# Kernel optimization log

Hardware: AMD Instinct MI355X
Metric: run time of the kernel (lower is better)

The kernel has to match this reference:

```python
import jax, jax.numpy as jnp
import numpy as np

NUM_HEADS = 8
CH_PER_HEAD = 32
NUM_GROUPS = 32
EPS = 1e-5
SCALE = CH_PER_HEAD ** (-0.25)


def group_norm(x, scale, bias):
    # x: [b, c, h, w]
    b, c, h, w = x.shape
    xg = x.reshape(b, NUM_GROUPS, c // NUM_GROUPS, h, w)
    mean = xg.mean(axis=(2, 3, 4), keepdims=True)
    var = xg.var(axis=(2, 3, 4), keepdims=True)
    xg = (xg - mean) * jax.lax.rsqrt(var + EPS)
    x = xg.reshape(b, c, h, w)
    return x * scale[None, :, None, None] + bias[None, :, None, None]


def conv1x1(x, w, b):
    # x: [b, c_in, n], w: [c_out, c_in], b: [c_out]
    return jnp.einsum('oc,bcn->bon', w, x) + b[None, :, None]


def setup_inputs() -> dict:
    key = jax.random.key(0)
    ks = jax.random.split(key, 12)
    c_in, c_out, hid = 256, 256, NUM_HEADS * CH_PER_HEAD
    d = {}
    d['x'] = jax.random.normal(ks[0], (2, c_in, 64, 64), dtype=jnp.float32)
    d['gn_scale'] = jnp.ones((c_in,), dtype=jnp.float32)
    d['gn_bias'] = jnp.zeros((c_in,), dtype=jnp.float32)
    def lin(k, co, ci):
        return jax.random.normal(k, (co, ci), dtype=jnp.float32) * (ci ** -0.5)
    d['wq'] = lin(ks[1], hid, c_in)
    d['bq'] = jnp.zeros((hid,), dtype=jnp.float32)
    d['wk'] = lin(ks[2], hid, c_in)
    d['bk'] = jnp.zeros((hid,), dtype=jnp.float32)
    d['wv'] = lin(ks[3], hid, c_in)
    d['bv'] = jnp.zeros((hid,), dtype=jnp.float32)
    # Original zero-inits to_out; we use small random weights so the
    # attention path contributes to the output (non-trivial baseline).
    d['wo'] = lin(ks[4], c_out, hid) * 0.02
    d['bo'] = jnp.zeros((c_out,), dtype=jnp.float32)
    return d


def reference(x, gn_scale, gn_bias, wq, bq, wk, bk, wv, bv, wo, bo):
    b, c, h, w = x.shape
    n = h * w
    x_n = group_norm(x, gn_scale, gn_bias).reshape(b, c, n)
    q = conv1x1(x_n, wq, bq)  # [b, hid, n]
    k = conv1x1(x_n, wk, bk)
    v = conv1x1(x_n, wv, bv)
    def split_heads(t):
        return t.reshape(b, NUM_HEADS, CH_PER_HEAD, n)
    q, k, v = split_heads(q) * SCALE, split_heads(k) * SCALE, split_heads(v)
    attn = jax.nn.softmax(jnp.einsum('bhdi,bhdj->bhij', q, k), axis=-1)
    out = jnp.einsum('bhij,bhdj->bhdi', attn, v)  # [b, h, d, n]
    out = out.reshape(b, NUM_HEADS * CH_PER_HEAD, n)
    out = conv1x1(out, wo, bo).reshape(b, -1, h, w)
    return x + out
```

## Files before the change

### kernel.cpp

```cpp
#include <hip/hip_runtime.h>

#define C 256
#define N 4096
#define CPG 8
#define GE (CPG * N)
#define JL 2048

constexpr float EPS = 1e-5f;
constexpr float QK_SCALE_E = 0.50500979f;

typedef float f32x4 __attribute__((ext_vector_type(4)));
typedef short s16x8 __attribute__((ext_vector_type(8)));

__device__ __forceinline__ short f2bf(float f) {
    union { float f; unsigned u; } v; v.f = f;
    unsigned r = v.u + 0x7FFFu + ((v.u >> 16) & 1u);
    return (short)(r >> 16);
}
__device__ __forceinline__ float bf2f(short s) {
    union { unsigned u; float f; } v; v.u = ((unsigned)(unsigned short)s) << 16;
    return v.f;
}

__global__ __launch_bounds__(256) void k_stats(const float* __restrict__ x,
                                               float2* __restrict__ partials) {
    int q = blockIdx.x & 3, g = (blockIdx.x >> 2) & 31, b = blockIdx.x >> 7;
    size_t base = (size_t)(b * C + g * CPG) * N + q * (GE / 4);
    const float* xp = x + base;
    int tid = threadIdx.x;
    float sum = 0.f, ss = 0.f;
    for (int i = tid * 4; i < GE / 4; i += 1024) {
        float4 v = *(const float4*)(xp + i);
        sum += (v.x + v.y) + (v.z + v.w);
        ss  += (v.x * v.x + v.y * v.y) + (v.z * v.z + v.w * v.w);
    }
    #pragma unroll
    for (int o = 32; o; o >>= 1) {
        sum += __shfl_down(sum, o, 64);
        ss  += __shfl_down(ss, o, 64);
    }
    __shared__ float red[8];
    int wid = tid >> 6;
    if ((tid & 63) == 0) { red[wid] = sum; red[4 + wid] = ss; }
    __syncthreads();
    if (tid == 0) {
        sum = red[0] + red[1] + red[2] + red[3];
        ss  = red[4] + red[5] + red[6] + red[7];
        partials[(b * 32 + g) * 4 + q] = make_float2(sum, ss);
    }
}

__global__ __launch_bounds__(256) void k_wcvt(const float* __restrict__ wq,
        const float* __restrict__ wk, const float* __restrict__ wv,
        const float* __restrict__ wo, short* __restrict__ wqkvb,
        short* __restrict__ wob) {
    int i = blockIdx.x * 256 + threadIdx.x;
    if (i < 65536)       wqkvb[i] = f2bf(wq[i]);
    else if (i < 131072) wqkvb[i] = f2bf(wk[i - 65536]);
    else if (i < 196608) wqkvb[i] = f2bf(wv[i - 131072]);
    else                 wob[i - 196608] = f2bf(wo[i - 196608]);
}

__global__ __launch_bounds__(256) void k_t(const float* __restrict__ x,
        const float* __restrict__ gs, const float* __restrict__ gb,
        const float2* __restrict__ partials, short* __restrict__ xnT) {
    __shared__ __align__(16) short lt[64][72];
    int id = blockIdx.x;
    int b  = id >> 8;
    int ct = (id >> 6) & 3;
    int nt = id & 63;
    int c0 = ct * 64, n0 = nt * 64;
    int t = threadIdx.x;
    int cc = t >> 2;
    int c = c0 + cc;
    int bg = b * 32 + (c >> 3);
    float2 p0 = partials[bg * 4 + 0], p1 = partials[bg * 4 + 1];
    float2 p2 = partials[bg * 4 + 2], p3 = partials[bg * 4 + 3];
    float sum = (p0.x + p1.x) + (p2.x + p3.x);
    float ss  = (p0.y + p1.y) + (p2.y + p3.y);
    float mean = sum * (1.f / GE);
    float var  = ss * (1.f / GE) - mean * mean;
    float rstd = rsqrtf(var + EPS);
    float sc = gs[c] * rstd;
    float bi = gb[c] - mean * sc;
    const float* xp = x + (size_t)(b * C + c) * N + n0;
    #pragma unroll
    for (int it = 0; it < 4; ++it) {
        int f4 = (t & 3) + it * 4;
        float4 v = *(const float4*)(xp + f4 * 4);
        int nl = f4 * 4;
        lt[nl + 0][cc] = f2bf(v.x * sc + bi);
        lt[nl + 1][cc] = f2bf(v.y * sc + bi);
        lt[nl + 2][cc] = f2bf(v.z * sc + bi);
        lt[nl + 3][cc] = f2bf(v.w * sc + bi);
    }
    __syncthreads();
    int nl = t >> 2, seg = t & 3;
    short* op = xnT + (size_t)(b * N + n0 + nl) * C + c0 + seg * 16;
    s16x8 w0 = *(const s16x8*)&lt[nl][seg * 16];
    s16x8 w1 = *(const s16x8*)&lt[nl][seg * 16 + 8];
    *(s16x8*)op = w0;
    *(s16x8*)(op + 8) = w1;
}

__global__ __launch_bounds__(256) void k_qkv(const short* __restrict__ wqkvb,
        const short* __restrict__ xnT, const float* __restrict__ bq,
        const float* __restrict__ bk, const float* __restrict__ bv,
        short* __restrict__ qT, short* __restrict__ kT, short* __restrict__ vB) {
    __shared__ __align__(16) short bs[64 * 256];
    __shared__ __align__(16) short lt[4][64][16];
    int mb = blockIdx.x, nb = blockIdx.y, b = blockIdx.z;
    int m0 = mb * 64, n0 = nb * 64;
    int t = threadIdx.x;
    int wid = t >> 6, lane = t & 63;
    int lr = lane & 15, lg = lane >> 4;
    int mw = m0 + wid * 16;

    const short* ap_ = wqkvb + (mw + lr) * C + lg * 8;
    s16x8 af[8];
    #pragma unroll
    for (int kk = 0; kk < 8; ++kk)
        af[kk] = *(const s16x8*)(ap_ + kk * 32);

    {
        int gr = t >> 2;
        const short* gp = xnT + ((size_t)b * N + n0 + gr) * C + (t & 3) * 8;
        #pragma unroll
        for (int i = 0; i < 8; ++i) {
            int sl = (t & 3) + 4 * i;
            s16x8 v = *(const s16x8*)(gp + 32 * i);
            *(s16x8*)&bs[gr * 256 + ((sl ^ (gr & 7)) * 8)] = v;
        }
    }
    __syncthreads();

    f32x4 acc[4] = {{0,0,0,0},{0,0,0,0},{0,0,0,0},{0,0,0,0}};
    #pragma unroll
    for (int kk = 0; kk < 8; ++kk) {
        int sb = kk * 4;
        #pragma unroll
        for (int f = 0; f < 4; ++f) {
            int row = f * 16 + lr;
            s16x8 xf = *(const s16x8*)&bs[row * 256 + (((sb + lg) ^ (lr & 7)) * 8)];
            acc[f] = __builtin_amdgcn_mfma_f32_16x16x32_bf16(af[kk], xf, acc[f], 0, 0, 0);
        }
    }

    int kind = mb >> 2;
    const float* bias = kind == 0 ? bq : (kind == 1 ? bk : bv);
    int mloc = mw - kind * 256;
    float bvals[4];
    #pragma unroll
    for (int r = 0; r < 4; ++r) bvals[r] = bias[mloc + 4 * lg + r];
    int h = mloc >> 5;
    if (kind == 2) {
        short (*vt)[64] = (short(*)[64])lt;
        #pragma unroll
        for (int f = 0; f < 4; ++f)
            #pragma unroll
            for (int r = 0; r < 4; ++r) {
                int rl = wid * 16 + 4 * lg + r;
                int cn = f * 16 + lr;
                int sl = cn >> 3, off = cn & 7;
                vt[rl][((sl ^ (rl & 7)) * 8) + off] = f2bf(acc[f][r] + bvals[r]);
            }
        __syncthreads();
        int mlocB = mb * 64 - 512;
        int h0 = mlocB >> 5;
        int rr = t >> 2, sl = t & 3;
        int h2 = h0 + (rr >> 5), dd = rr & 31;
        short* vdst = vB + ((size_t)((b * 8 + h2) * 32 + dd)) * N + n0;
        s16x8 w0v = *(const s16x8*)&vt[rr][(sl ^ (rr & 7)) * 8];
        s16x8 w1v = *(const s16x8*)&vt[rr][((sl + 4) ^ (rr & 7)) * 8];
        *(s16x8*)(vdst + sl * 8) = w0v;
        *(s16x8*)(vdst + (sl + 4) * 8) = w1v;
    } else {
        short* dst = (kind == 0) ? qT : kT;
        #pragma unroll
        for (int f = 0; f < 4; ++f)
            #pragma unroll
            for (int r = 0; r < 4; ++r)
                lt[wid][f * 16 + lr][4 * lg + r] =
                    f2bf((acc[f][r] + bvals[r]) * QK_SCALE_E);
        int ln = lane;
        s16x8 w0 = *(const s16x8*)&lt[wid][ln][0];
        s16x8 w1 = *(const s16x8*)&lt[wid][ln][8];
        short* op = dst + ((size_t)(b * 8 + h) * N + n0 + ln) * 32 + (mloc & 16);
        *(s16x8*)op = w0;
        *(s16x8*)(op + 8) = w1;
    }
}

#define EXPB(d, s_) asm("v_exp_f32 %0, %1\n\ts_nop 0" : "=v"(d) : "v"(s_))

#define TILE_BODY() do {                                                          \
    f32x4 s0 = __builtin_amdgcn_mfma_f32_16x16x32_bf16(bk0, aq, zero, 0, 0, 0);   \
    f32x4 s1 = __builtin_amdgcn_mfma_f32_16x16x32_bf16(bk1, aq, zero, 0, 0, 0);   \
    float e00, e01, e02, e03, e10, e11, e12, e13;                                 \
    EXPB(e00, s0[0]); EXPB(e01, s0[1]); EXPB(e02, s0[2]); EXPB(e03, s0[3]);       \
    EXPB(e10, s1[0]); EXPB(e11, s1[1]); EXPB(e12, s1[2]); EXPB(e13, s1[3]);       \
    unsigned w0, w1, w2, w3;                                                      \
    asm("v_cvt_pk_bf16_f32 %0, %1, %2" : "=v"(w0) : "v"(e00), "v"(e01));          \
    asm("v_cvt_pk_bf16_f32 %0, %1, %2" : "=v"(w1) : "v"(e02), "v"(e03));          \
    asm("v_cvt_pk_bf16_f32 %0, %1, %2" : "=v"(w2) : "v"(e10), "v"(e11));          \
    asm("v_cvt_pk_bf16_f32 %0, %1, %2" : "=v"(w3) : "v"(e12), "v"(e13));          \
    asm("v_permlane32_swap_b32 %0, %1" : "+v"(w0), "+v"(w2));                     \
    asm("v_permlane16_swap_b32 %0, %1" : "+v"(w0), "+v"(w2));                     \
    asm("v_permlane32_swap_b32 %0, %1" : "+v"(w1), "+v"(w3));                     \
    asm("v_permlane16_swap_b32 %0, %1" : "+v"(w1), "+v"(w3));                     \
    union { int4 i4; s16x8 s8; } apu;                                             \
    apu.i4 = make_int4((int)w0, (int)w1, (int)w2, (int)w3);                       \
    s16x8 ap = apu.s8;                                                            \
    lac = __builtin_amdgcn_mfma_f32_16x16x32_bf16(ap, ones, lac, 0, 0, 0);        \
    o0  = __builtin_amdgcn_mfma_f32_16x16x32_bf16(ap, bv0, o0, 0, 0, 0);          \
    o1  = __builtin_amdgcn_mfma_f32_16x16x32_bf16(ap, bv1, o1, 0, 0, 0);          \
} while (0)

__global__ __launch_bounds__(256, 8) void k_attn(const short* __restrict__ qT,
        const short* __restrict__ kT, const short* __restrict__ vB,
        short* __restrict__ po0, short* __restrict__ po1,
        float* __restrict__ pl) {
    __shared__ __align__(16) short pool[8192];
    int xb  = blockIdx.x;
    int rm  = (xb & 7) * 128 + (xb >> 3);
    int bh  = rm >> 6;
    int wid = threadIdx.x >> 6;
    int i0  = (rm & 63) * 64 + wid * 16;
    int s   = blockIdx.y;
    int jb  = s * JL;
    int lane = threadIdx.x & 63;
    int lr = lane & 15, lg = lane >> 4;
    const short* qTb = qT + (size_t)bh * N * 32;
    const short* kTb = kT + (size_t)bh * N * 32;
    const short* vBb = vB + (size_t)bh * 32 * N;

    s16x8 aq = *(const s16x8*)(qTb + (i0 + lr) * 32 + lg * 8);
    s16x8 ones;
    #pragma unroll
    for (int e = 0; e < 8; ++e) ones[e] = (short)0x3F80;

    f32x4 o0 = {0,0,0,0}, o1 = {0,0,0,0}, lac = {0,0,0,0};
    const f32x4 zero = {0,0,0,0};

    int krow  = 16 * wid + (lane >> 2);
    int kslot = lane & 3;
    const short* kg = kTb + (size_t)(jb + krow) * 32 + kslot * 8;
    int kw_ofs = krow * 32 + ((kslot ^ (krow & 3)) * 8);

    int vrow  = 8 * wid + (lane >> 3);
    int vslot = lane & 7;
    const short* vg = vBb + (size_t)vrow * N + jb + vslot * 8;
    int vw_ofs = vrow * 64 + ((vslot ^ (vrow & 7)) * 8);

    int kr_base = lr * 32 + ((lg ^ (lr & 3)) * 8);
    int vr0 = lr * 64, vr1 = (16 + lr) * 64;
    int sw0 = ((0 + lg) ^ (lr & 7)) * 8;
    int sw1 = ((4 + lg) ^ (lr & 7)) * 8;

    {
        s16x8 kreg = *(const s16x8*)kg;
        s16x8 vreg = *(const s16x8*)vg;
        *(s16x8*)&pool[kw_ofs] = kreg;
        *(s16x8*)&pool[4096 + vw_ofs] = vreg;
    }
    __syncthreads();

    for (int t = 0; t < 32; ++t) {
        int p = t & 1;
        s16x8 nk, nv;
        if (t < 31) {
            nk = *(const s16x8*)(kg + (t + 1) * 2048);
            nv = *(const s16x8*)(vg + (t + 1) * 64);
        }
        const short* lkp = &pool[p * 2048];
        const short* lvp = &pool[4096 + p * 2048];
        {
            s16x8 bk0 = *(const s16x8*)(lkp + kr_base);
            s16x8 bk1 = *(const s16x8*)(lkp + 512 + kr_base);
            s16x8 bv0 = *(const s16x8*)(lvp + vr0 + sw0);
            s16x8 bv1 = *(const s16x8*)(lvp + vr1 + sw0);
            TILE_BODY();
        }
        {
            s16x8 bk0 = *(const s16x8*)(lkp + 1024 + kr_base);
            s16x8 bk1 = *(const s16x8*)(lkp + 1536 + kr_base);
            s16x8 bv0 = *(const s16x8*)(lvp + vr0 + sw1);
            s16x8 bv1 = *(const s16x8*)(lvp + vr1 + sw1);
            TILE_BODY();
        }
        if (t < 31) {
            int q = (t + 1) & 1;
            *(s16x8*)&pool[q * 2048 + kw_ofs] = nk;
            *(s16x8*)&pool[4096 + q * 2048 + vw_ofs] = nv;
        }
        __syncthreads();
    }

    #pragma unroll
    for (int r = 0; r < 4; ++r) {
        pool[wid * 640 + (4 * lg + r) * 40 + lr]      = f2bf(o0[r]);
        pool[wid * 640 + (4 * lg + r) * 40 + 16 + lr] = f2bf(o1[r]);
    }
    if (lr == 0) {
        float* plp = pl + ((size_t)(s * 16 + bh)) * N + i0;
        #pragma unroll
        for (int r = 0; r < 4; ++r) plp[4 * lg + r] = lac[r];
    }
    short* pob = s ? po1 : po0;
    int il = lane >> 2, seg = lane & 3;
    s16x8 w = *(const s16x8*)&pool[wid * 640 + il * 40 + seg * 8];
    short* op = pob + ((size_t)bh * N + i0 + il) * 32 + seg * 8;
    *(s16x8*)op = w;
}

__global__ __launch_bounds__(256) void k_out(const short* __restrict__ wob,
        const short* __restrict__ po0, const short* __restrict__ po1,
        const float* __restrict__ pl, const float* __restrict__ bo,
        const float* __restrict__ x, float* __restrict__ out) {
    __shared__ __align__(16) short bs[8 * 32 * 32];
    int mb = blockIdx.x, nb = blockIdx.y, b = blockIdx.z;
    int n0 = nb * 32;
    int t = threadIdx.x;
    int wid = t >> 6, lane = t & 63;
    int lr = lane & 15, lg = lane >> 4;
    int mw = mb * 64 + wid * 16;

    const short* ap_ = wob + (mw + lr) * C + lg * 8;
    s16x8 af[8];
    #pragma unroll
    for (int h = 0; h < 8; ++h) af[h] = *(const s16x8*)(ap_ + h * 32);

    {
        int h = t >> 5, idx = t & 31;
        size_t rb = ((size_t)(b * 8 + h)) * N + n0;
        const short* g0 = po0 + rb * 32;
        const short* g1 = po1 + rb * 32;
        const float* pl0 = pl + rb;
        const float* pl1 = pl + ((size_t)(16 + b * 8 + h)) * N + n0;
        #pragma unroll
        for (int i = 0; i < 4; ++i) {
            int chunk = idx + 32 * i;
            int r = chunk >> 2, sl = chunk & 3;
            s16x8 v0 = *(const s16x8*)(g0 + r * 32 + sl * 8);
            s16x8 v1 = *(const s16x8*)(g1 + r * 32 + sl * 8);
            float inv = 1.f / (pl0[r] + pl1[r]);
            s16x8 w;
            #pragma unroll
            for (int e = 0; e < 8; ++e)
                w[e] = f2bf((bf2f(v0[e]) + bf2f(v1[e])) * inv);
            *(s16x8*)&bs[h * 1024 + r * 32 + ((sl ^ (r & 3)) * 8)] = w;
        }
    }
    __syncthreads();

    f32x4 acc[2] = {{0,0,0,0},{0,0,0,0}};
    #pragma unroll
    for (int h = 0; h < 8; ++h) {
        #pragma unroll
        for (int f = 0; f < 2; ++f) {
            int row = f * 16 + lr;
            s16x8 xf = *(const s16x8*)&bs[h * 1024 + row * 32 + ((lg ^ (lr & 3)) * 8)];
            acc[f] = __builtin_amdgcn_mfma_f32_16x16x32_bf16(af[h], xf, acc[f], 0, 0, 0);
        }
    }

    float bvals[4];
    #pragma unroll
    for (int r = 0; r < 4; ++r) bvals[r] = bo[mw + 4 * lg + r];
    #pragma unroll
    for (int f = 0; f < 2; ++f) {
        int n = n0 + f * 16 + lr;
        #pragma unroll
        for (int r = 0; r < 4; ++r) {
            size_t idx = (size_t)(b * C + mw + 4 * lg + r) * N + n;
            out[idx] = acc[f][r] + bvals[r] + x[idx];
        }
    }
}

extern "C" void kernel_launch(void* const* d_in, const int* in_sizes, int n_in,
                              void* d_out, int out_size, void* d_ws, size_t ws_size,
                              hipStream_t stream) {
    const float* x  = (const float*)d_in[0];
    const float* gs = (const float*)d_in[1];
    const float* gb = (const float*)d_in[2];
    const float* wq = (const float*)d_in[3];
    const float* bq = (const float*)d_in[4];
    const float* wk = (const float*)d_in[5];
    const float* bk = (const float*)d_in[6];
    const float* wv = (const float*)d_in[7];
    const float* bv = (const float*)d_in[8];
    const float* wo = (const float*)d_in[9];
    const float* bo = (const float*)d_in[10];
    float* out = (float*)d_out;
    char* ws = (char*)d_ws;

    float2* partials = (float2*)(ws);
    short*  wqkvb = (short*)(ws + 0x1000);
    float*  pl    = (float*)(ws + 0x1000);
    short*  wob   = (short*)(ws + 0x81000);
    short*  xnT   = (short*)(ws + 0xB0000);
    short*  po1   = (short*)(ws + 0xB0000);
    short*  qT    = (short*)(ws + 0x4B0000);
    short*  kT    = (short*)(ws + 0x8B0000);
    short*  vB    = (short*)(ws + 0xCB0000);
    short*  po0   = (short*)(ws + 0x10B0000);

    k_stats<<<256, 256, 0, stream>>>(x, partials);
    k_wcvt <<<1024, 256, 0, stream>>>(wq, wk, wv, wo, wqkvb, wob);
    k_t    <<<512, 256, 0, stream>>>(x, gs, gb, partials, xnT);
    k_qkv  <<<dim3(12, 64, 2), 256, 0, stream>>>(wqkvb, xnT, bq, bk, bv, qT, kT, vB);
    k_attn <<<dim3(1024, 2), 256, 0, stream>>>(qT, kT, vB, po0, po1, pl);
    k_out  <<<dim3(4, 128, 2), 256, 0, stream>>>(wob, po0, po1, pl, bo, x, out);
}
```

Baseline: 158.8 us.

## Merge stats and weight-convert kernels, reuse LDS in qkv, raise attn MFMA priority

The group-norm statistics kernel and the weight bf16 conversion kernel are merged into one launch, with the block index choosing the role, to save a kernel launch. The qkv kernel drops its separate staging buffer and reuses the operand LDS area after an added barrier, which lowers LDS use and may let more blocks fit per CU. The attention inner loop raises wave priority around the MFMA/exp section with s_setprio. Each change is small, and the extra barrier adds some sync cost.

```diff
diff --git a/kernel.cpp b/kernel.cpp
--- a/kernel.cpp
+++ b/kernel.cpp
@@ -22,43 +22,43 @@
     return v.f;
 }
 
-__global__ __launch_bounds__(256) void k_stats(const float* __restrict__ x,
-                                               float2* __restrict__ partials) {
-    int q = blockIdx.x & 3, g = (blockIdx.x >> 2) & 31, b = blockIdx.x >> 7;
-    size_t base = (size_t)(b * C + g * CPG) * N + q * (GE / 4);
-    const float* xp = x + base;
-    int tid = threadIdx.x;
-    float sum = 0.f, ss = 0.f;
-    for (int i = tid * 4; i < GE / 4; i += 1024) {
-        float4 v = *(const float4*)(xp + i);
-        sum += (v.x + v.y) + (v.z + v.w);
-        ss  += (v.x * v.x + v.y * v.y) + (v.z * v.z + v.w * v.w);
-    }
-    #pragma unroll
-    for (int o = 32; o; o >>= 1) {
-        sum += __shfl_down(sum, o, 64);
-        ss  += __shfl_down(ss, o, 64);
-    }
-    __shared__ float red[8];
-    int wid = tid >> 6;
-    if ((tid & 63) == 0) { red[wid] = sum; red[4 + wid] = ss; }
-    __syncthreads();
-    if (tid == 0) {
-        sum = red[0] + red[1] + red[2] + red[3];
-        ss  = red[4] + red[5] + red[6] + red[7];
-        partials[(b * 32 + g) * 4 + q] = make_float2(sum, ss);
-    }
-}
-
-__global__ __launch_bounds__(256) void k_wcvt(const float* __restrict__ wq,
-        const float* __restrict__ wk, const float* __restrict__ wv,
-        const float* __restrict__ wo, short* __restrict__ wqkvb,
+__global__ __launch_bounds__(256) void k_prep(const float* __restrict__ x,
+        const float* __restrict__ wq, const float* __restrict__ wk,
+        const float* __restrict__ wv, const float* __restrict__ wo,
+        float2* __restrict__ partials, short* __restrict__ wqkvb,
         short* __restrict__ wob) {
-    int i = blockIdx.x * 256 + threadIdx.x;
-    if (i < 65536)       wqkvb[i] = f2bf(wq[i]);
-    else if (i < 131072) wqkvb[i] = f2bf(wk[i - 65536]);
-    else if (i < 196608) wqkvb[i] = f2bf(wv[i - 131072]);
-    else                 wob[i - 196608] = f2bf(wo[i - 196608]);
+    if (blockIdx.x < 256) {
+        int q = blockIdx.x & 3, g = (blockIdx.x >> 2) & 31, b = (int)blockIdx.x >> 7;
+        size_t base = (size_t)(b * C + g * CPG) * N + q * (GE / 4);
+        const float* xp = x + base;
+        int tid = threadIdx.x;
+        float sum = 0.f, ss = 0.f;
+        for (int i = tid * 4; i < GE / 4; i += 1024) {
+            float4 v = *(const float4*)(xp + i);
+            sum += (v.x + v.y) + (v.z + v.w);
+            ss  += (v.x * v.x + v.y * v.y) + (v.z * v.z + v.w * v.w);
+        }
+        #pragma unroll
+        for (int o = 32; o; o >>= 1) {
+            sum += __shfl_down(sum, o, 64);
+            ss  += __shfl_down(ss, o, 64);
+        }
+        __shared__ float red[8];
+        int wid = tid >> 6;
+        if ((tid & 63) == 0) { red[wid] = sum; red[4 + wid] = ss; }
+        __syncthreads();
+        if (tid == 0) {
+            sum = red[0] + red[1] + red[2] + red[3];
+            ss  = red[4] + red[5] + red[6] + red[7];
+            partials[(b * 32 + g) * 4 + q] = make_float2(sum, ss);
+        }
+    } else {
+        int i = (blockIdx.x - 256) * 256 + threadIdx.x;
+        if (i < 65536)       wqkvb[i] = f2bf(wq[i]);
+        else if (i < 131072) wqkvb[i] = f2bf(wk[i - 65536]);
+        else if (i < 196608) wqkvb[i] = f2bf(wv[i - 131072]);
+        else                 wob[i - 196608] = f2bf(wo[i - 196608]);
+    }
 }
 
 __global__ __launch_bounds__(256) void k_t(const float* __restrict__ x,
@@ -108,7 +108,6 @@
         const float* __restrict__ bk, const float* __restrict__ bv,
         short* __restrict__ qT, short* __restrict__ kT, short* __restrict__ vB) {
     __shared__ __align__(16) short bs[64 * 256];
-    __shared__ __align__(16) short lt[4][64][16];
     int mb = blockIdx.x, nb = blockIdx.y, b = blockIdx.z;
     int m0 = mb * 64, n0 = nb * 64;
     int t = threadIdx.x;
@@ -145,6 +144,7 @@
             acc[f] = __builtin_amdgcn_mfma_f32_16x16x32_bf16(af[kk], xf, acc[f], 0, 0, 0);
         }
     }
+    __syncthreads();
 
     int kind = mb >> 2;
     const float* bias = kind == 0 ? bq : (kind == 1 ? bk : bv);
@@ -154,7 +154,7 @@
     for (int r = 0; r < 4; ++r) bvals[r] = bias[mloc + 4 * lg + r];
     int h = mloc >> 5;
     if (kind == 2) {
-        short (*vt)[64] = (short(*)[64])lt;
+        short (*vt)[64] = (short(*)[64])bs;
         #pragma unroll
         for (int f = 0; f < 4; ++f)
             #pragma unroll
@@ -175,16 +175,17 @@
         *(s16x8*)(vdst + sl * 8) = w0v;
         *(s16x8*)(vdst + (sl + 4) * 8) = w1v;
     } else {
+        short (*ltw)[16] = (short(*)[16])&bs[wid * 1024];
         short* dst = (kind == 0) ? qT : kT;
         #pragma unroll
         for (int f = 0; f < 4; ++f)
             #pragma unroll
             for (int r = 0; r < 4; ++r)
-                lt[wid][f * 16 + lr][4 * lg + r] =
+                ltw[f * 16 + lr][4 * lg + r] =
                     f2bf((acc[f][r] + bvals[r]) * QK_SCALE_E);
         int ln = lane;
-        s16x8 w0 = *(const s16x8*)&lt[wid][ln][0];
-        s16x8 w1 = *(const s16x8*)&lt[wid][ln][8];
+        s16x8 w0 = *(const s16x8*)&ltw[ln][0];
+        s16x8 w1 = *(const s16x8*)&ltw[ln][8];
         short* op = dst + ((size_t)(b * 8 + h) * N + n0 + ln) * 32 + (mloc & 16);
         *(s16x8*)op = w0;
         *(s16x8*)(op + 8) = w1;
@@ -274,6 +275,7 @@
         }
         const short* lkp = &pool[p * 2048];
         const short* lvp = &pool[4096 + p * 2048];
+        __builtin_amdgcn_s_setprio(1);
         {
             s16x8 bk0 = *(const s16x8*)(lkp + kr_base);
             s16x8 bk1 = *(const s16x8*)(lkp + 512 + kr_base);
@@ -288,6 +290,7 @@
             s16x8 bv1 = *(const s16x8*)(lvp + vr1 + sw1);
             TILE_BODY();
         }
+        __builtin_amdgcn_s_setprio(0);
         if (t < 31) {
             int q = (t + 1) & 1;
             *(s16x8*)&pool[q * 2048 + kw_ofs] = nk;
@@ -406,8 +409,7 @@
     short*  vB    = (short*)(ws + 0xCB0000);
     short*  po0   = (short*)(ws + 0x10B0000);
 
-    k_stats<<<256, 256, 0, stream>>>(x, partials);
-    k_wcvt <<<1024, 256, 0, stream>>>(wq, wk, wv, wo, wqkvb, wob);
+    k_prep <<<1280, 256, 0, stream>>>(x, wq, wk, wv, wo, partials, wqkvb, wob);
     k_t    <<<512, 256, 0, stream>>>(x, gs, gb, partials, xnT);
     k_qkv  <<<dim3(12, 64, 2), 256, 0, stream>>>(wqkvb, xnT, bq, bk, bv, qT, kT, vB);
     k_attn <<<dim3(1024, 2), 256, 0, stream>>>(qT, kT, vB, po0, po1, pl);
```

Result: slower. 163.1 us (+2.7%).
